# Optimization experiments

Measured on AMD Instinct MI355X. Metric: run time of the kernel, lower is better.

## Reference

```python
import jax, jax.numpy as jnp
from jax import lax
import numpy as np

SCORE_THRESH = 0.05
NMS_THRESH = 0.5
MAX_DET = 100
MIN_SIZE = 0.01
BBOX_CLIP = float(np.log(1000.0 / 16.0))
NEG = -1e10


def setup_inputs() -> dict:
    key = jax.random.key(0)
    ks = jax.random.split(key, 12)
    N, IN, REP, C = 2000, 256 * 7 * 7, 1024, 91
    box_features = jax.random.normal(ks[0], (N, IN), jnp.float32)
    x1 = jax.random.uniform(ks[1], (N,), jnp.float32, 0.0, 1000.0)
    y1 = jax.random.uniform(ks[2], (N,), jnp.float32, 0.0, 600.0)
    bw = jax.random.uniform(ks[3], (N,), jnp.float32, 16.0, 200.0)
    bh = jax.random.uniform(ks[4], (N,), jnp.float32, 16.0, 180.0)
    proposals = jnp.stack([x1, y1, x1 + bw, y1 + bh], axis=1)
    W1 = jax.random.normal(ks[5], (IN, REP), jnp.float32) * 0.01
    b1 = jnp.zeros((REP,), jnp.float32)
    W2 = jax.random.normal(ks[6], (REP, REP), jnp.float32) * 0.03
    b2 = jnp.zeros((REP,), jnp.float32)
    Wc = jax.random.normal(ks[7], (REP, C), jnp.float32) * 0.1
    bc = jax.random.normal(ks[8], (C,), jnp.float32) * 0.5
    Wr = jax.random.normal(ks[9], (REP, 4 * C), jnp.float32) * 0.01
    br = jnp.zeros((4 * C,), jnp.float32)
    return dict(box_features=box_features, proposals=proposals,
                W1=W1, b1=b1, W2=W2, b2=b2, Wc=Wc, bc=bc, Wr=Wr, br=br,
                image_h=800, image_w=1216)


def _nms(boxes, scores):
    """Greedy NMS with fixed trip count; scores already masked to NEG for invalid."""
    M = boxes.shape[0]
    areas = (boxes[:, 2] - boxes[:, 0]) * (boxes[:, 3] - boxes[:, 1])
    idxs = jnp.arange(M)

    def step(sm, _):
        i = jnp.argmax(sm)
        valid = sm[i] > NEG * 0.5
        b = boxes[i]
        xx1 = jnp.maximum(b[0], boxes[:, 0]); yy1 = jnp.maximum(b[1], boxes[:, 1])
        xx2 = jnp.minimum(b[2], boxes[:, 2]); yy2 = jnp.minimum(b[3], boxes[:, 3])
        inter = jnp.clip(xx2 - xx1, 0.0) * jnp.clip(yy2 - yy1, 0.0)
        iou = inter / (areas[i] + areas - inter + 1e-9)
        suppress = (iou > NMS_THRESH) | (idxs == i)
        sm = jnp.where(valid, jnp.where(suppress, NEG, sm), sm)
        return sm, jnp.where(valid, i, -1)

    _, keep = lax.scan(step, scores, None, length=MAX_DET)
    return keep  # [MAX_DET] int, -1 for padding


def reference(box_features, proposals, W1, b1, W2, b2, Wc, bc, Wr, br, image_h, image_w):
    N = box_features.shape[0]
    C = Wc.shape[1]
    # box head MLP (Linear+ReLU x2) and predictors
    h = jax.nn.relu(box_features @ W1 + b1)
    h = jax.nn.relu(h @ W2 + b2)
    class_logits = h @ Wc + bc                      # [N, C]
    box_reg = (h @ Wr + br).reshape(N, C, 4)        # [N, C, 4]
    # box decode (weights 10,10,5,5) against proposals
    pw = proposals[:, 2] - proposals[:, 0]
    ph = proposals[:, 3] - proposals[:, 1]
    pcx = proposals[:, 0] + 0.5 * pw
    pcy = proposals[:, 1] + 0.5 * ph
    dx = box_reg[..., 0] / 10.0
    dy = box_reg[..., 1] / 10.0
    dw = jnp.minimum(box_reg[..., 2] / 5.0, BBOX_CLIP)
    dh = jnp.minimum(box_reg[..., 3] / 5.0, BBOX_CLIP)
    cx = dx * pw[:, None] + pcx[:, None]
    cy = dy * ph[:, None] + pcy[:, None]
    w = jnp.exp(dw) * pw[:, None]
    hh = jnp.exp(dh) * ph[:, None]
    boxes = jnp.stack([cx - 0.5 * w, cy - 0.5 * hh, cx + 0.5 * w, cy + 0.5 * hh], axis=-1)
    scores = jax.nn.softmax(class_logits, axis=-1)
    # clip to image
    Wim = jnp.float32(image_w); Him = jnp.float32(image_h)
    boxes = jnp.stack([jnp.clip(boxes[..., 0], 0.0, Wim),
                       jnp.clip(boxes[..., 1], 0.0, Him),
                       jnp.clip(boxes[..., 2], 0.0, Wim),
                       jnp.clip(boxes[..., 3], 0.0, Him)], axis=-1)
    # drop background class, flatten to [N*(C-1)]
    boxes = boxes[:, 1:].reshape(-1, 4)
    scores = scores[:, 1:].reshape(-1)
    labels = jnp.broadcast_to(jnp.arange(1, C, dtype=jnp.int32), (N, C - 1)).reshape(-1)
    # score threshold + remove small boxes (as masking, static shapes)
    bw = boxes[:, 2] - boxes[:, 0]
    bh = boxes[:, 3] - boxes[:, 1]
    valid = (scores > SCORE_THRESH) & (bw >= MIN_SIZE) & (bh >= MIN_SIZE)
    sm = jnp.where(valid, scores, NEG)
    # class-aware (batched) NMS via per-class coordinate offsets
    off = labels.astype(boxes.dtype) * (jnp.maximum(Wim, Him) + 1.0)
    keep = _nms(boxes + off[:, None], sm)
    mask = keep >= 0
    idx = jnp.maximum(keep, 0)
    out_boxes = jnp.take(boxes, idx, axis=0) * mask[:, None]
    out_scores = jnp.take(scores, idx) * mask
    out_labels = jnp.take(labels, idx) * mask.astype(jnp.int32)
    return out_boxes, out_scores, out_labels
```

## Files before the change

kernel.cpp:

```cpp
#include <hip/hip_runtime.h>

#define CPC 2000
#define SPC 100
#define NCLS 90
#define TM 128
#define TN 128
#define TKK 16

typedef __attribute__((ext_vector_type(8))) short bf16x8;
typedef __attribute__((ext_vector_type(4))) float f32x4;

__device__ __forceinline__ unsigned short f2bf_rne(float f) {
    unsigned u = __float_as_uint(f);
    return (unsigned short)((u + 0x7FFFu + ((u >> 16) & 1u)) >> 16);
}
__device__ __forceinline__ unsigned short f2bf_trunc(float f) {
    return (unsigned short)(__float_as_uint(f) >> 16);
}
__device__ __forceinline__ float bfhi_f32(float f) {
    return __uint_as_float(__float_as_uint(f) & 0xFFFF0000u);
}
__device__ __forceinline__ void async_load16(const void* g, void* l) {
    __builtin_amdgcn_global_load_lds((const __attribute__((address_space(1))) unsigned int*)g,
                                     (__attribute__((address_space(3))) unsigned int*)l, 16, 0, 0);
}
__device__ __forceinline__ int swz(int c) { return c ^ ((c >> 3) & 3); }

__global__ __launch_bounds__(256) void split_transpose(
    const float* __restrict__ W, unsigned short* __restrict__ Thi,
    unsigned short* __restrict__ Tlo, int K, int N)
{
    __shared__ float tile[32][33];
    const int kt = blockIdx.x * 32, nt = blockIdx.y * 32;
    const int tx = threadIdx.x & 31, ty = threadIdx.x >> 5;
#pragma unroll
    for (int j = 0; j < 4; ++j) {
        int k = kt + ty + j * 8, n = nt + tx;
        tile[ty + j * 8][tx] = (k < K && n < N) ? W[(size_t)k * N + n] : 0.f;
    }
    __syncthreads();
#pragma unroll
    for (int j = 0; j < 4; ++j) {
        int n = nt + ty + j * 8, k = kt + tx;
        if (n < N && k < K) {
            float f = tile[tx][ty + j * 8];
            Thi[(size_t)n * K + k] = f2bf_trunc(f);
            Tlo[(size_t)n * K + k] = f2bf_rne(f - bfhi_f32(f));
        }
    }
}

__global__ __launch_bounds__(256) void split_transpose2(
    const float* __restrict__ Wa, const float* __restrict__ Wb, int Na, int Nb,
    unsigned short* __restrict__ Thi, unsigned short* __restrict__ Tlo, int K)
{
    const int N = Na + Nb;
    __shared__ float tile[32][33];
    const int kt = blockIdx.x * 32, nt = blockIdx.y * 32;
    const int tx = threadIdx.x & 31, ty = threadIdx.x >> 5;
#pragma unroll
    for (int j = 0; j < 4; ++j) {
        int k = kt + ty + j * 8, n = nt + tx;
        float v = 0.f;
        if (k < K && n < N)
            v = (n < Na) ? Wa[(size_t)k * Na + n] : Wb[(size_t)k * Nb + (n - Na)];
        tile[ty + j * 8][tx] = v;
    }
    __syncthreads();
#pragma unroll
    for (int j = 0; j < 4; ++j) {
        int n = nt + ty + j * 8, k = kt + tx;
        if (n < N && k < K) {
            float f = tile[tx][ty + j * 8];
            Thi[(size_t)n * K + k] = f2bf_trunc(f);
            Tlo[(size_t)n * K + k] = f2bf_rne(f - bfhi_f32(f));
        }
    }
}

__global__ __launch_bounds__(256, 4) void gemm_bf16x3_f32a(
    const float* __restrict__ A, const unsigned short* __restrict__ Bhi,
    const unsigned short* __restrict__ Blo, float* __restrict__ C,
    int M, int N, int K, int klen)
{
    __shared__ unsigned short Ah[2048], Al[2048], Bh[4096], Bl[4096];
    const int tid = threadIdx.x;
    const int wv = tid >> 6, ln = tid & 63;
    const int q = ln >> 4, lm = ln & 15;
    const int m0 = blockIdx.y * 64, n0 = blockIdx.x * 128;
    const int k0 = blockIdx.z * klen, k1 = k0 + klen;
    const int bcol_t = wv * 32;

    f32x4 acc[4][2];
#pragma unroll
    for (int i = 0; i < 4; ++i)
#pragma unroll
        for (int j = 0; j < 2; ++j) acc[i][j] = (f32x4)0.f;

    const int r = tid >> 2, h = tid & 3;
    int gr = m0 + r; if (gr >= M) gr = M - 1;
    const float* Arow = A + (size_t)gr * K + h * 8;
    const int apc = swz(tid);

    unsigned bsrc[2];
#pragma unroll
    for (int i = 0; i < 2; ++i) {
        int s = i * 256 + tid;
        int gn = n0 + (s >> 2); if (gn >= N) gn = N - 1;
        int qe = (s & 3) ^ ((s >> 3) & 3);
        bsrc[i] = (unsigned)gn * (unsigned)K + (unsigned)(qe * 8);
    }

    for (int kt = k0; kt < k1; kt += 32) {
#pragma unroll
        for (int i = 0; i < 2; ++i) {
            async_load16(Bhi + bsrc[i] + kt, &Bh[(i * 256 + wv * 64) * 8]);
            async_load16(Blo + bsrc[i] + kt, &Bl[(i * 256 + wv * 64) * 8]);
        }
        float4 v0 = *reinterpret_cast<const float4*>(Arow + kt);
        float4 v1 = *reinterpret_cast<const float4*>(Arow + kt + 4);
        float f[8] = {v0.x, v0.y, v0.z, v0.w, v1.x, v1.y, v1.z, v1.w};
        bf16x8 hi, lo;
#pragma unroll
        for (int e = 0; e < 8; ++e) {
            hi[e] = (short)f2bf_trunc(f[e]);
            lo[e] = (short)f2bf_rne(f[e] - bfhi_f32(f[e]));
        }
        *(bf16x8*)&Ah[apc * 8] = hi;
        *(bf16x8*)&Al[apc * 8] = lo;
        __syncthreads();

        bf16x8 afh[4], afl[4], bfh[2], bfl[2];
#pragma unroll
        for (int mi = 0; mi < 4; ++mi) {
            int p = swz((mi * 16 + lm) * 4 + q);
            afh[mi] = *(const bf16x8*)&Ah[p * 8];
            afl[mi] = *(const bf16x8*)&Al[p * 8];
        }
#pragma unroll
        for (int ni = 0; ni < 2; ++ni) {
            int p = swz((bcol_t + ni * 16 + lm) * 4 + q);
            bfh[ni] = *(const bf16x8*)&Bh[p * 8];
            bfl[ni] = *(const bf16x8*)&Bl[p * 8];
        }
#pragma unroll
        for (int mi = 0; mi < 4; ++mi)
#pragma unroll
            for (int ni = 0; ni < 2; ++ni) {
                acc[mi][ni] = __builtin_amdgcn_mfma_f32_16x16x32_bf16(afh[mi], bfh[ni], acc[mi][ni], 0, 0, 0);
                acc[mi][ni] = __builtin_amdgcn_mfma_f32_16x16x32_bf16(afl[mi], bfh[ni], acc[mi][ni], 0, 0, 0);
                acc[mi][ni] = __builtin_amdgcn_mfma_f32_16x16x32_bf16(afh[mi], bfl[ni], acc[mi][ni], 0, 0, 0);
            }
        __syncthreads();
    }

    float* Cz = C + (size_t)blockIdx.z * (size_t)M * (size_t)N;
#pragma unroll
    for (int mi = 0; mi < 4; ++mi)
#pragma unroll
        for (int ni = 0; ni < 2; ++ni)
#pragma unroll
            for (int ri = 0; ri < 4; ++ri) {
                int rr = m0 + mi * 16 + q * 4 + ri;
                int cc = n0 + bcol_t + ni * 16 + lm;
                if (rr < M && cc < N) Cz[(size_t)rr * N + cc] = acc[mi][ni][ri];
            }
}

__global__ __launch_bounds__(256, 4) void gemm_bf16x3_sa(
    const unsigned short* __restrict__ Ahi_g, const unsigned short* __restrict__ Alo_g,
    const unsigned short* __restrict__ Bhi, const unsigned short* __restrict__ Blo,
    float* __restrict__ C, int M, int N, int K, int klen)
{
    __shared__ unsigned short Ah[2048], Al[2048], Bh[4096], Bl[4096];
    const int tid = threadIdx.x;
    const int wv = tid >> 6, ln = tid & 63;
    const int q = ln >> 4, lm = ln & 15;
    const int m0 = blockIdx.y * 64, n0 = blockIdx.x * 128;
    const int k0 = blockIdx.z * klen, k1 = k0 + klen;
    const int bcol_t = wv * 32;

    f32x4 acc[4][2];
#pragma unroll
    for (int i = 0; i < 4; ++i)
#pragma unroll
        for (int j = 0; j < 2; ++j) acc[i][j] = (f32x4)0.f;

    {
    }
    int agr = m0 + (tid >> 2); if (agr >= M) agr = M - 1;
    const int aqe = (tid & 3) ^ ((tid >> 3) & 3);
    const unsigned asrc = (unsigned)agr * (unsigned)K + (unsigned)(aqe * 8);

    unsigned bsrc[2];
#pragma unroll
    for (int i = 0; i < 2; ++i) {
        int s = i * 256 + tid;
        int gn = n0 + (s >> 2); if (gn >= N) gn = N - 1;
        int qe = (s & 3) ^ ((s >> 3) & 3);
        bsrc[i] = (unsigned)gn * (unsigned)K + (unsigned)(qe * 8);
    }

    for (int kt = k0; kt < k1; kt += 32) {
        async_load16(Ahi_g + asrc + kt, &Ah[(wv * 64) * 8]);
        async_load16(Alo_g + asrc + kt, &Al[(wv * 64) * 8]);
#pragma unroll
        for (int i = 0; i < 2; ++i) {
            async_load16(Bhi + bsrc[i] + kt, &Bh[(i * 256 + wv * 64) * 8]);
            async_load16(Blo + bsrc[i] + kt, &Bl[(i * 256 + wv * 64) * 8]);
        }
        __syncthreads();

        bf16x8 afh[4], afl[4], bfh[2], bfl[2];
#pragma unroll
        for (int mi = 0; mi < 4; ++mi) {
            int p = swz((mi * 16 + lm) * 4 + q);
            afh[mi] = *(const bf16x8*)&Ah[p * 8];
            afl[mi] = *(const bf16x8*)&Al[p * 8];
        }
#pragma unroll
        for (int ni = 0; ni < 2; ++ni) {
            int p = swz((bcol_t + ni * 16 + lm) * 4 + q);
            bfh[ni] = *(const bf16x8*)&Bh[p * 8];
            bfl[ni] = *(const bf16x8*)&Bl[p * 8];
        }
#pragma unroll
        for (int mi = 0; mi < 4; ++mi)
#pragma unroll
            for (int ni = 0; ni < 2; ++ni) {
                acc[mi][ni] = __builtin_amdgcn_mfma_f32_16x16x32_bf16(afh[mi], bfh[ni], acc[mi][ni], 0, 0, 0);
                acc[mi][ni] = __builtin_amdgcn_mfma_f32_16x16x32_bf16(afl[mi], bfh[ni], acc[mi][ni], 0, 0, 0);
                acc[mi][ni] = __builtin_amdgcn_mfma_f32_16x16x32_bf16(afh[mi], bfl[ni], acc[mi][ni], 0, 0, 0);
            }
        __syncthreads();
    }

    float* Cz = C + (size_t)blockIdx.z * (size_t)M * (size_t)N;
#pragma unroll
    for (int mi = 0; mi < 4; ++mi)
#pragma unroll
        for (int ni = 0; ni < 2; ++ni)
#pragma unroll
            for (int ri = 0; ri < 4; ++ri) {
                int rr = m0 + mi * 16 + q * 4 + ri;
                int cc = n0 + bcol_t + ni * 16 + lm;
                if (rr < M && cc < N) Cz[(size_t)rr * N + cc] = acc[mi][ni][ri];
            }
}

__global__ __launch_bounds__(256) void gemm_f32(
    const float* __restrict__ A, const float* __restrict__ B,
    const float* __restrict__ bias, float* __restrict__ C,
    int M, int N, int K, int ksplit, int relu)
{
    __shared__ float As[TKK][TM + 4];
    __shared__ float Bs[TKK][TN + 4];
    const int tid = threadIdx.x;
    const int tx = tid & 15, ty = tid >> 4;
    const int m0 = blockIdx.y * TM, n0 = blockIdx.x * TN;
    const int z = blockIdx.z;
    const int kstart = z * ksplit;
    const int kend = (kstart + ksplit < K) ? (kstart + ksplit) : K;
    float* Cz = C + (size_t)z * (size_t)M * (size_t)N;
    const bool nvec = ((N & 3) == 0);

    float acc[8][8];
#pragma unroll
    for (int i = 0; i < 8; ++i)
#pragma unroll
        for (int j = 0; j < 8; ++j) acc[i][j] = 0.f;

    for (int kt = kstart; kt < kend; kt += TKK) {
#pragma unroll
        for (int l = 0; l < 2; ++l) {
            int idx = tid + l * 256;
            int rr = idx >> 2, kq = idx & 3;
            float4 v = make_float4(0.f, 0.f, 0.f, 0.f);
            int grr = m0 + rr;
            if (grr < M)
                v = *reinterpret_cast<const float4*>(A + (size_t)grr * K + kt + (kq << 2));
            As[(kq << 2) + 0][rr] = v.x;
            As[(kq << 2) + 1][rr] = v.y;
            As[(kq << 2) + 2][rr] = v.z;
            As[(kq << 2) + 3][rr] = v.w;
        }
#pragma unroll
        for (int l = 0; l < 2; ++l) {
            int idx = tid + l * 256;
            int kk = idx >> 5, nq = idx & 31;
            int gn = n0 + (nq << 2);
            const float* bp = B + (size_t)(kt + kk) * N + gn;
            float4 v;
            if (nvec && gn + 3 < N) {
                v = *reinterpret_cast<const float4*>(bp);
            } else {
                v.x = (gn + 0 < N) ? bp[0] : 0.f;
                v.y = (gn + 1 < N) ? bp[1] : 0.f;
                v.z = (gn + 2 < N) ? bp[2] : 0.f;
                v.w = (gn + 3 < N) ? bp[3] : 0.f;
            }
            *reinterpret_cast<float4*>(&Bs[kk][nq << 2]) = v;
        }
        __syncthreads();
#pragma unroll
        for (int kk = 0; kk < TKK; ++kk) {
            float a[8], b[8];
            *reinterpret_cast<float4*>(&a[0]) = *reinterpret_cast<const float4*>(&As[kk][ty * 8]);
            *reinterpret_cast<float4*>(&a[4]) = *reinterpret_cast<const float4*>(&As[kk][ty * 8 + 4]);
            *reinterpret_cast<float4*>(&b[0]) = *reinterpret_cast<const float4*>(&Bs[kk][tx * 4]);
            *reinterpret_cast<float4*>(&b[4]) = *reinterpret_cast<const float4*>(&Bs[kk][64 + tx * 4]);
#pragma unroll
            for (int i = 0; i < 8; ++i)
#pragma unroll
                for (int j = 0; j < 8; ++j)
                    acc[i][j] = fmaf(a[i], b[j], acc[i][j]);
        }
        __syncthreads();
    }
#pragma unroll
    for (int i = 0; i < 8; ++i) {
        int grr = m0 + ty * 8 + i;
        if (grr >= M) continue;
#pragma unroll
        for (int j = 0; j < 8; ++j) {
            int gc = n0 + ((j < 4) ? (tx * 4 + j) : (64 + tx * 4 + (j - 4)));
            if (gc >= N) continue;
            float v = acc[i][j];
            if (bias) v += bias[gc];
            if (relu) v = fmaxf(v, 0.f);
            Cz[(size_t)grr * N + gc] = v;
        }
    }
}

__global__ void combine_bias_act(const float* __restrict__ P, const float* __restrict__ bias,
                                 float* __restrict__ H, int total, int N, int nsplit,
                                 int pstride, int relu)
{
    int i = blockIdx.x * blockDim.x + threadIdx.x;
    if (i >= total) return;
    float s = P[i];
    for (int j = 1; j < nsplit; ++j) s += P[i + (size_t)j * (size_t)pstride];
    s += bias[i % N];
    if (relu) s = fmaxf(s, 0.f);
    H[i] = s;
}

__global__ void combine_bias_split(const float* __restrict__ P, const float* __restrict__ bias,
                                   unsigned short* __restrict__ Hhi, unsigned short* __restrict__ Hlo,
                                   int total, int N, int nsplit, int pstride, int relu)
{
    int i = blockIdx.x * blockDim.x + threadIdx.x;
    if (i >= total) return;
    float s = P[i];
    for (int j = 1; j < nsplit; ++j) s += P[i + (size_t)j * (size_t)pstride];
    s += bias[i % N];
    if (relu) s = fmaxf(s, 0.f);
    Hhi[i] = f2bf_trunc(s);
    Hlo[i] = f2bf_rne(s - bfhi_f32(s));
}

__global__ void combine_head(const float* __restrict__ P, const float* __restrict__ bc,
                             const float* __restrict__ br, float* __restrict__ H,
                             int total, int nsplit, int pstride)
{
    int i = blockIdx.x * blockDim.x + threadIdx.x;
    if (i >= total) return;
    float s = P[i];
    for (int j = 1; j < nsplit; ++j) s += P[i + (size_t)j * (size_t)pstride];
    int col = i % 455;
    s += (col < 91) ? bc[col] : br[col - 91];
    H[i] = s;
}

__device__ __forceinline__ float scalar_dim(const int* p)
{
    int iv = *p;
    return (iv > 0 && iv < (1 << 20)) ? (float)iv : *reinterpret_cast<const float*>(p);
}

__global__ __launch_bounds__(128) void decode_compact(
    const float* __restrict__ logits, int lstr, const float* __restrict__ breg, int bstr,
    const float4* __restrict__ proposals, const int* __restrict__ ihp,
    const int* __restrict__ iwp,
    float4* __restrict__ cbox, float* __restrict__ cscore, int* __restrict__ cn,
    int* __restrict__ ccnt)
{
    const int n = blockIdx.x;
    const int c = threadIdx.x;
    __shared__ float sl[91];
    __shared__ float s_max, s_sum;
    if (c < 91) sl[c] = logits[(size_t)n * lstr + c];
    __syncthreads();
    if (c == 0) {
        float m = sl[0];
        for (int i = 1; i < 91; ++i) m = fmaxf(m, sl[i]);
        float s = 0.f;
        for (int i = 0; i < 91; ++i) s += expf(sl[i] - m);
        s_max = m; s_sum = s;
    }
    __syncthreads();
    if (c < 1 || c >= 91) return;

    const float score = expf(sl[c] - s_max) / s_sum;
    const float Wim = scalar_dim(iwp), Him = scalar_dim(ihp);
    float4 p = proposals[n];
    float pw = p.z - p.x, ph = p.w - p.y;
    float pcx = p.x + 0.5f * pw, pcy = p.y + 0.5f * ph;
    const float* r4 = breg + (size_t)n * bstr + c * 4;
    float dxv = r4[0] / 10.f, dyv = r4[1] / 10.f;
    const float BCLIP = 4.135166556742356f;
    float dwv = fminf(r4[2] / 5.f, BCLIP);
    float dhv = fminf(r4[3] / 5.f, BCLIP);
    float cx = dxv * pw + pcx, cy = dyv * ph + pcy;
    float w = expf(dwv) * pw, hh = expf(dhv) * ph;
    float x1 = cx - 0.5f * w, y1 = cy - 0.5f * hh;
    float x2 = cx + 0.5f * w, y2 = cy + 0.5f * hh;
    x1 = fminf(fmaxf(x1, 0.f), Wim);
    y1 = fminf(fmaxf(y1, 0.f), Him);
    x2 = fminf(fmaxf(x2, 0.f), Wim);
    y2 = fminf(fmaxf(y2, 0.f), Him);
    float bw = x2 - x1, bh = y2 - y1;
    if (score > 0.05f && bw >= 0.01f && bh >= 0.01f) {
        int cls = c - 1;
        int pos = atomicAdd(&ccnt[cls], 1);
        if (pos < CPC) {
            cbox[cls * CPC + pos] = make_float4(x1, y1, x2, y2);
            cscore[cls * CPC + pos] = score;
            cn[cls * CPC + pos] = n;
        }
    }
}

__global__ __launch_bounds__(256) void nms_class(
    const float4* __restrict__ cbox, const float* __restrict__ cscore,
    const int* __restrict__ cn, const int* __restrict__ ccnt,
    float4* __restrict__ sbox, float* __restrict__ sscore,
    unsigned long long* __restrict__ skey, int* __restrict__ scnt)
{
    const int cls = blockIdx.x;
    const int tid = threadIdx.x;
    int cnt = ccnt[cls]; if (cnt > CPC) cnt = CPC;

    __shared__ float4 cb[CPC];
    __shared__ unsigned long long keys[CPC];
    __shared__ unsigned long long red[4];
    __shared__ float4 selsh;
    __shared__ int selidx_sh;

    for (int i = tid; i < cnt; i += 256) {
        cb[i] = cbox[cls * CPC + i];
        unsigned int sb = __float_as_uint(cscore[cls * CPC + i]);
        sb ^= (sb >> 31) ? 0xFFFFFFFFu : 0x80000000u;
        unsigned int flat = (unsigned)cn[cls * CPC + i] * 90u + (unsigned)cls;
        keys[i] = ((unsigned long long)sb << 32) | (unsigned long long)(0xFFFFFFFFu - flat);
    }
    __syncthreads();

    int sel = 0;
    while (sel < SPC) {
        unsigned long long best = 0ull;
        for (int i = tid; i < cnt; i += 256) {
            unsigned long long k = keys[i];
            if (k > best) best = k;
        }
#pragma unroll
        for (int d = 32; d >= 1; d >>= 1) {
            unsigned long long o = __shfl_down(best, d, 64);
            if (o > best) best = o;
        }
        if ((tid & 63) == 0) red[tid >> 6] = best;
        __syncthreads();
        unsigned long long gbest = red[0];
        if (red[1] > gbest) gbest = red[1];
        if (red[2] > gbest) gbest = red[2];
        if (red[3] > gbest) gbest = red[3];
        if (gbest == 0ull) break;
        for (int i = tid; i < cnt; i += 256)
            if (keys[i] == gbest) { selsh = cb[i]; selidx_sh = i; }
        __syncthreads();
        float4 s = selsh;
        const int si = selidx_sh;
        const float sa = (s.z - s.x) * (s.w - s.y);
        if (tid == 0) {
            sbox[cls * SPC + sel] = s;
            unsigned int sb = (unsigned int)(gbest >> 32);
            sb ^= (sb >> 31) ? 0x80000000u : 0xFFFFFFFFu;
            sscore[cls * SPC + sel] = __uint_as_float(sb);
            skey[cls * SPC + sel] = gbest;
        }
        for (int i = tid; i < cnt; i += 256) {
            float4 b = cb[i];
            float xx1 = fmaxf(s.x, b.x), yy1 = fmaxf(s.y, b.y);
            float xx2 = fminf(s.z, b.z), yy2 = fminf(s.w, b.w);
            float inter = fmaxf(xx2 - xx1, 0.f) * fmaxf(yy2 - yy1, 0.f);
            float area = (b.z - b.x) * (b.w - b.y);
            if (3.f * inter > sa + area + 1e-9f || i == si) keys[i] = 0ull;
        }
        ++sel;
        __syncthreads();
    }
    if (tid == 0) scnt[cls] = sel;
}

__global__ __launch_bounds__(128) void nms_merge(
    const float4* __restrict__ sbox, const float* __restrict__ sscore,
    const unsigned long long* __restrict__ skey, const int* __restrict__ scnt,
    float* __restrict__ out)
{
    const int tid = threadIdx.x;
    __shared__ int head[NCLS];
    __shared__ unsigned long long red[2];
    __shared__ int selc_sh;
    if (tid < NCLS) head[tid] = 0;
    __syncthreads();

    for (int k = 0; k < 100; ++k) {
        unsigned long long key = 0ull;
        if (tid < NCLS && head[tid] < scnt[tid]) key = skey[tid * SPC + head[tid]];
        unsigned long long mykey = key;
#pragma unroll
        for (int d = 32; d >= 1; d >>= 1) {
            unsigned long long o = __shfl_down(key, d, 64);
            if (o > key) key = o;
        }
        if ((tid & 63) == 0) red[tid >> 6] = key;
        if (tid == 0) selc_sh = -1;
        __syncthreads();
        unsigned long long gbest = red[0] > red[1] ? red[0] : red[1];
        if (gbest != 0ull && mykey == gbest) selc_sh = tid;
        __syncthreads();
        const int c = selc_sh;
        if (tid == 0) {
            if (c >= 0) {
                int h = head[c];
                float4 b = sbox[c * SPC + h];
                out[k * 4 + 0] = b.x; out[k * 4 + 1] = b.y;
                out[k * 4 + 2] = b.z; out[k * 4 + 3] = b.w;
                out[400 + k] = sscore[c * SPC + h];
                out[500 + k] = (float)(c + 1);
            } else {
                out[k * 4 + 0] = 0.f; out[k * 4 + 1] = 0.f;
                out[k * 4 + 2] = 0.f; out[k * 4 + 3] = 0.f;
                out[400 + k] = 0.f; out[500 + k] = 0.f;
            }
        }
        if (c >= 0 && tid == c) head[c]++;
        __syncthreads();
    }
}

extern "C" void kernel_launch(void* const* d_in, const int* in_sizes, int n_in,
                              void* d_out, int out_size, void* d_ws, size_t ws_size,
                              hipStream_t stream)
{
    const float* bf    = (const float*)d_in[0];
    const float* props = (const float*)d_in[1];
    const float* W1    = (const float*)d_in[2];
    const float* b1    = (const float*)d_in[3];
    const float* W2    = (const float*)d_in[4];
    const float* b2    = (const float*)d_in[5];
    const float* Wc    = (const float*)d_in[6];
    const float* bc    = (const float*)d_in[7];
    const float* Wr    = (const float*)d_in[8];
    const float* br    = (const float*)d_in[9];
    const int*   ihp   = (const int*)d_in[10];
    const int*   iwp   = (const int*)d_in[11];
    float* ws  = (float*)d_ws;
    float* out = (float*)d_out;

    const size_t MN   = 2000ull * 1024ull;
    const size_t NLOG = 2000ull * 91ull;
    const size_t NREG = 2000ull * 364ull;
    const size_t NHEAD = 2000ull * 455ull;
    const size_t ws_floats = ws_size / 4;

    const size_t BT1F = 1024ull * 12544ull / 2;
    const size_t WT2F = 1024ull * 1024ull / 2;
    const size_t WHF  = 455ull * 1024ull / 2;
    const size_t NMSF = (size_t)NCLS * CPC * 6 + (size_t)NCLS * SPC * 7 + 256;
    const size_t PF   = 4 * MN;
    const size_t NEED = 2 * BT1F + 2 * WT2F + 2 * WHF + 2 * MN + NHEAD + NMSF + PF + 64;

    if (ws_floats >= NEED) {
        unsigned short* BT1hi = (unsigned short*)ws;
        unsigned short* BT1lo = (unsigned short*)(ws + BT1F);
        unsigned short* WT2hi = (unsigned short*)(ws + 2 * BT1F);
        unsigned short* WT2lo = (unsigned short*)(ws + 2 * BT1F + WT2F);
        unsigned short* WHhi  = (unsigned short*)(ws + 2 * BT1F + 2 * WT2F);
        unsigned short* WHlo  = (unsigned short*)(ws + 2 * BT1F + 2 * WT2F + WHF);
        float* H1   = ws + 2 * BT1F + 2 * WT2F + 2 * WHF;
        float* H2   = H1 + MN;
        float* HEAD = H2 + MN;
        float* CBOX   = HEAD + NHEAD;
        float* CSCORE = CBOX + (size_t)NCLS * CPC * 4;
        int*   CN     = (int*)(CSCORE + (size_t)NCLS * CPC);
        float* SBOX   = (float*)(CN + (size_t)NCLS * CPC);
        float* SSCORE = SBOX + (size_t)NCLS * SPC * 4;
        unsigned long long* SKEY = (unsigned long long*)(SSCORE + (size_t)NCLS * SPC);
        int*   CCNT = (int*)(SKEY + (size_t)NCLS * SPC);
        int*   SCNT = CCNT + NCLS;
        float* P = (float*)(SCNT + NCLS + 62);

        unsigned short* H1hi = (unsigned short*)H1;
        unsigned short* H1lo = H1hi + MN;
        unsigned short* H2hi = (unsigned short*)H2;
        unsigned short* H2lo = H2hi + MN;

        split_transpose<<<dim3(392, 32), 256, 0, stream>>>(W1, BT1hi, BT1lo, 12544, 1024);
        split_transpose<<<dim3(32, 32), 256, 0, stream>>>(W2, WT2hi, WT2lo, 1024, 1024);
        split_transpose2<<<dim3(32, 15), 256, 0, stream>>>(Wc, Wr, 91, 364, WHhi, WHlo, 1024);
        gemm_bf16x3_f32a<<<dim3(8, 32, 4), 256, 0, stream>>>(bf, BT1hi, BT1lo, P,
                                                             2000, 1024, 12544, 3136);
        combine_bias_split<<<(int)((MN + 255) / 256), 256, 0, stream>>>(P, b1, H1hi, H1lo,
                                                             (int)MN, 1024, 4, (int)MN, 1);
        gemm_bf16x3_sa<<<dim3(8, 32, 4), 256, 0, stream>>>(H1hi, H1lo, WT2hi, WT2lo, P,
                                                           2000, 1024, 1024, 256);
        combine_bias_split<<<(int)((MN + 255) / 256), 256, 0, stream>>>(P, b2, H2hi, H2lo,
                                                             (int)MN, 1024, 4, (int)MN, 1);
        gemm_bf16x3_sa<<<dim3(4, 32, 8), 256, 0, stream>>>(H2hi, H2lo, WHhi, WHlo, P,
                                                           2000, 455, 1024, 128);
        combine_head<<<(int)((NHEAD + 255) / 256), 256, 0, stream>>>(P, bc, br, HEAD,
                                                             (int)NHEAD, 8, (int)NHEAD);
        hipMemsetAsync(CCNT, 0, 2 * NCLS * sizeof(int), stream);
        decode_compact<<<2000, 128, 0, stream>>>(HEAD, 455, HEAD + 91, 455,
                                                 (const float4*)props, ihp, iwp,
                                                 (float4*)CBOX, CSCORE, CN, CCNT);
        nms_class<<<NCLS, 256, 0, stream>>>((const float4*)CBOX, CSCORE, CN, CCNT,
                                            (float4*)SBOX, SSCORE, SKEY, SCNT);
        nms_merge<<<1, 128, 0, stream>>>((const float4*)SBOX, SSCORE, SKEY, SCNT, out);
        return;
    }

    const size_t NMSF2 = (size_t)NCLS * CPC * 6 + (size_t)NCLS * SPC * 7 + 256;
    const size_t TAILF = 2 * MN + NLOG + NREG + NMSF2;
    int z1 = 2;
    if (ws_floats >= TAILF + 8 * MN) z1 = 8;
    else if (ws_floats >= TAILF + 4 * MN) z1 = 4;
    const size_t REUSE = (size_t)z1 * MN;
    int zh = (REUSE >= 8 * NREG) ? 8 : 4;

    float* P      = ws;
    float* H1     = P + REUSE;
    float* H2     = H1 + MN;
    float* LOG    = H2 + MN;
    float* BREG   = LOG + NLOG;
    float* CBOX   = BREG + NREG;
    float* CSCORE = CBOX + (size_t)NCLS * CPC * 4;
    int*   CN     = (int*)(CSCORE + (size_t)NCLS * CPC);
    float* SBOX   = (float*)(CN + (size_t)NCLS * CPC);
    float* SSCORE = SBOX + (size_t)NCLS * SPC * 4;
    unsigned long long* SKEY = (unsigned long long*)(SSCORE + (size_t)NCLS * SPC);
    int*   CCNT   = (int*)(SKEY + (size_t)NCLS * SPC);
    int*   SCNT   = CCNT + NCLS;

    gemm_f32<<<dim3(8, 16, z1), 256, 0, stream>>>(bf, W1, nullptr, P,
                                                  2000, 1024, 12544, 12544 / z1, 0);
    combine_bias_act<<<(int)((MN + 255) / 256), 256, 0, stream>>>(P, b1, H1,
                                                  (int)MN, 1024, z1, (int)MN, 1);
    gemm_f32<<<dim3(8, 16, 4), 256, 0, stream>>>(H1, W2, nullptr, P,
                                                 2000, 1024, 1024, 256, 0);
    combine_bias_act<<<(int)((MN + 255) / 256), 256, 0, stream>>>(P, b2, H2,
                                                 (int)MN, 1024, 4, (int)MN, 1);
    gemm_f32<<<dim3(1, 16, zh), 256, 0, stream>>>(H2, Wc, nullptr, P,
                                                  2000, 91, 1024, 1024 / zh, 0);
    combine_bias_act<<<(int)((NLOG + 255) / 256), 256, 0, stream>>>(P, bc, LOG,
                                                  (int)NLOG, 91, zh, (int)NLOG, 0);
    gemm_f32<<<dim3(3, 16, zh), 256, 0, stream>>>(H2, Wr, nullptr, P,
                                                  2000, 364, 1024, 1024 / zh, 0);
    combine_bias_act<<<(int)((NREG + 255) / 256), 256, 0, stream>>>(P, br, BREG,
                                                  (int)NREG, 364, zh, (int)NREG, 0);
    hipMemsetAsync(CCNT, 0, 2 * NCLS * sizeof(int), stream);
    decode_compact<<<2000, 128, 0, stream>>>(LOG, 91, BREG, 364,
                                             (const float4*)props, ihp, iwp,
                                             (float4*)CBOX, CSCORE, CN, CCNT);
    nms_class<<<NCLS, 256, 0, stream>>>((const float4*)CBOX, CSCORE, CN, CCNT,
                                        (float4*)SBOX, SSCORE, SKEY, SCNT);
    nms_merge<<<1, 128, 0, stream>>>((const float4*)SBOX, SSCORE, SKEY, SCNT, out);
}
```

Measured before the change: 751.0 us.

## Retune split-K counts, vectorize combine/transposes, raise GEMM occupancy, parallelize softmax

Changes the split-K factors of the three GEMMs (6, 5 and 6 splits with a clamped k1) and raises the launch bounds from 4 to 6 blocks per SM. The transpose-split kernels now handle 64 k-rows per block and write packed pairs of bf16 values. The combine kernels load and store float4 vectors. The softmax max/sum in decode moves from a single thread to tree reductions in shared memory. Workspace buffers are aliased so they fit the larger partial-sum buffers, and it is easy to get the liveness of these aliases wrong. The higher launch bound can also force register spills.

```diff
diff --git a/kernel.cpp b/kernel.cpp
--- a/kernel.cpp
+++ b/kernel.cpp
@@ -9,6 +9,7 @@
 
 typedef __attribute__((ext_vector_type(8))) short bf16x8;
 typedef __attribute__((ext_vector_type(4))) float f32x4;
+typedef __attribute__((ext_vector_type(4))) unsigned short u16x4;
 
 __device__ __forceinline__ unsigned short f2bf_rne(float f) {
     unsigned u = __float_as_uint(f);
@@ -30,22 +31,27 @@
     const float* __restrict__ W, unsigned short* __restrict__ Thi,
     unsigned short* __restrict__ Tlo, int K, int N)
 {
-    __shared__ float tile[32][33];
-    const int kt = blockIdx.x * 32, nt = blockIdx.y * 32;
+    __shared__ float tile[64][33];
+    const int kt = blockIdx.x * 64, nt = blockIdx.y * 32;
     const int tx = threadIdx.x & 31, ty = threadIdx.x >> 5;
 #pragma unroll
-    for (int j = 0; j < 4; ++j) {
+    for (int j = 0; j < 8; ++j) {
         int k = kt + ty + j * 8, n = nt + tx;
         tile[ty + j * 8][tx] = (k < K && n < N) ? W[(size_t)k * N + n] : 0.f;
     }
     __syncthreads();
 #pragma unroll
     for (int j = 0; j < 4; ++j) {
-        int n = nt + ty + j * 8, k = kt + tx;
+        int n = nt + ty + j * 8;
+        int k = kt + tx * 2;
         if (n < N && k < K) {
-            float f = tile[tx][ty + j * 8];
-            Thi[(size_t)n * K + k] = f2bf_trunc(f);
-            Tlo[(size_t)n * K + k] = f2bf_rne(f - bfhi_f32(f));
+            float f0 = tile[tx * 2][ty + j * 8];
+            float f1 = tile[tx * 2 + 1][ty + j * 8];
+            unsigned hi = (unsigned)f2bf_trunc(f0) | ((unsigned)f2bf_trunc(f1) << 16);
+            unsigned lo = (unsigned)f2bf_rne(f0 - bfhi_f32(f0))
+                        | ((unsigned)f2bf_rne(f1 - bfhi_f32(f1)) << 16);
+            *reinterpret_cast<unsigned*>(&Thi[(size_t)n * K + k]) = hi;
+            *reinterpret_cast<unsigned*>(&Tlo[(size_t)n * K + k]) = lo;
         }
     }
 }
@@ -55,11 +61,11 @@
     unsigned short* __restrict__ Thi, unsigned short* __restrict__ Tlo, int K)
 {
     const int N = Na + Nb;
-    __shared__ float tile[32][33];
-    const int kt = blockIdx.x * 32, nt = blockIdx.y * 32;
+    __shared__ float tile[64][33];
+    const int kt = blockIdx.x * 64, nt = blockIdx.y * 32;
     const int tx = threadIdx.x & 31, ty = threadIdx.x >> 5;
 #pragma unroll
-    for (int j = 0; j < 4; ++j) {
+    for (int j = 0; j < 8; ++j) {
         int k = kt + ty + j * 8, n = nt + tx;
         float v = 0.f;
         if (k < K && n < N)
@@ -69,16 +75,21 @@
     __syncthreads();
 #pragma unroll
     for (int j = 0; j < 4; ++j) {
-        int n = nt + ty + j * 8, k = kt + tx;
+        int n = nt + ty + j * 8;
+        int k = kt + tx * 2;
         if (n < N && k < K) {
-            float f = tile[tx][ty + j * 8];
-            Thi[(size_t)n * K + k] = f2bf_trunc(f);
-            Tlo[(size_t)n * K + k] = f2bf_rne(f - bfhi_f32(f));
-        }
-    }
-}
-
-__global__ __launch_bounds__(256, 4) void gemm_bf16x3_f32a(
+            float f0 = tile[tx * 2][ty + j * 8];
+            float f1 = tile[tx * 2 + 1][ty + j * 8];
+            unsigned hi = (unsigned)f2bf_trunc(f0) | ((unsigned)f2bf_trunc(f1) << 16);
+            unsigned lo = (unsigned)f2bf_rne(f0 - bfhi_f32(f0))
+                        | ((unsigned)f2bf_rne(f1 - bfhi_f32(f1)) << 16);
+            *reinterpret_cast<unsigned*>(&Thi[(size_t)n * K + k]) = hi;
+            *reinterpret_cast<unsigned*>(&Tlo[(size_t)n * K + k]) = lo;
+        }
+    }
+}
+
+__global__ __launch_bounds__(256, 6) void gemm_bf16x3_f32a(
     const float* __restrict__ A, const unsigned short* __restrict__ Bhi,
     const unsigned short* __restrict__ Blo, float* __restrict__ C,
     int M, int N, int K, int klen)
@@ -88,7 +99,8 @@
     const int wv = tid >> 6, ln = tid & 63;
     const int q = ln >> 4, lm = ln & 15;
     const int m0 = blockIdx.y * 64, n0 = blockIdx.x * 128;
-    const int k0 = blockIdx.z * klen, k1 = k0 + klen;
+    const int k0 = blockIdx.z * klen;
+    int k1 = k0 + klen; if (k1 > K) k1 = K;
     const int bcol_t = wv * 32;
 
     f32x4 acc[4][2];
@@ -97,9 +109,8 @@
 #pragma unroll
         for (int j = 0; j < 2; ++j) acc[i][j] = (f32x4)0.f;
 
-    const int r = tid >> 2, h = tid & 3;
-    int gr = m0 + r; if (gr >= M) gr = M - 1;
-    const float* Arow = A + (size_t)gr * K + h * 8;
+    int gr = m0 + (tid >> 2); if (gr >= M) gr = M - 1;
+    const float* Arow = A + (size_t)gr * K + (tid & 3) * 8;
     const int apc = swz(tid);
 
     unsigned bsrc[2];
@@ -167,7 +178,7 @@
             }
 }
 
-__global__ __launch_bounds__(256, 4) void gemm_bf16x3_sa(
+__global__ __launch_bounds__(256, 6) void gemm_bf16x3_sa(
     const unsigned short* __restrict__ Ahi_g, const unsigned short* __restrict__ Alo_g,
     const unsigned short* __restrict__ Bhi, const unsigned short* __restrict__ Blo,
     float* __restrict__ C, int M, int N, int K, int klen)
@@ -177,7 +188,8 @@
     const int wv = tid >> 6, ln = tid & 63;
     const int q = ln >> 4, lm = ln & 15;
     const int m0 = blockIdx.y * 64, n0 = blockIdx.x * 128;
-    const int k0 = blockIdx.z * klen, k1 = k0 + klen;
+    const int k0 = blockIdx.z * klen;
+    int k1 = k0 + klen; if (k1 > K) k1 = K;
     const int bcol_t = wv * 32;
 
     f32x4 acc[4][2];
@@ -186,11 +198,9 @@
 #pragma unroll
         for (int j = 0; j < 2; ++j) acc[i][j] = (f32x4)0.f;
 
-    {
-    }
     int agr = m0 + (tid >> 2); if (agr >= M) agr = M - 1;
-    const int aqe = (tid & 3) ^ ((tid >> 3) & 3);
-    const unsigned asrc = (unsigned)agr * (unsigned)K + (unsigned)(aqe * 8);
+    const unsigned asrc = (unsigned)agr * (unsigned)K
+                        + (unsigned)(((tid & 3) ^ ((tid >> 3) & 3)) * 8);
 
     unsigned bsrc[2];
 #pragma unroll
@@ -350,27 +360,44 @@
                                    unsigned short* __restrict__ Hhi, unsigned short* __restrict__ Hlo,
                                    int total, int N, int nsplit, int pstride, int relu)
 {
-    int i = blockIdx.x * blockDim.x + threadIdx.x;
+    int i = (blockIdx.x * blockDim.x + threadIdx.x) * 4;
     if (i >= total) return;
-    float s = P[i];
-    for (int j = 1; j < nsplit; ++j) s += P[i + (size_t)j * (size_t)pstride];
-    s += bias[i % N];
-    if (relu) s = fmaxf(s, 0.f);
-    Hhi[i] = f2bf_trunc(s);
-    Hlo[i] = f2bf_rne(s - bfhi_f32(s));
+    float4 s = *reinterpret_cast<const float4*>(P + i);
+    for (int j = 1; j < nsplit; ++j) {
+        float4 p = *reinterpret_cast<const float4*>(P + i + (size_t)j * (size_t)pstride);
+        s.x += p.x; s.y += p.y; s.z += p.z; s.w += p.w;
+    }
+    const float4 b = *reinterpret_cast<const float4*>(bias + (i % N));
+    s.x += b.x; s.y += b.y; s.z += b.z; s.w += b.w;
+    if (relu) {
+        s.x = fmaxf(s.x, 0.f); s.y = fmaxf(s.y, 0.f);
+        s.z = fmaxf(s.z, 0.f); s.w = fmaxf(s.w, 0.f);
+    }
+    u16x4 hi = { f2bf_trunc(s.x), f2bf_trunc(s.y), f2bf_trunc(s.z), f2bf_trunc(s.w) };
+    u16x4 lo = { f2bf_rne(s.x - bfhi_f32(s.x)), f2bf_rne(s.y - bfhi_f32(s.y)),
+                 f2bf_rne(s.z - bfhi_f32(s.z)), f2bf_rne(s.w - bfhi_f32(s.w)) };
+    *reinterpret_cast<u16x4*>(&Hhi[i]) = hi;
+    *reinterpret_cast<u16x4*>(&Hlo[i]) = lo;
 }
 
 __global__ void combine_head(const float* __restrict__ P, const float* __restrict__ bc,
                              const float* __restrict__ br, float* __restrict__ H,
                              int total, int nsplit, int pstride)
 {
-    int i = blockIdx.x * blockDim.x + threadIdx.x;
+    int i = (blockIdx.x * blockDim.x + threadIdx.x) * 4;
     if (i >= total) return;
-    float s = P[i];
-    for (int j = 1; j < nsplit; ++j) s += P[i + (size_t)j * (size_t)pstride];
-    int col = i % 455;
-    s += (col < 91) ? bc[col] : br[col - 91];
-    H[i] = s;
+    float4 s = *reinterpret_cast<const float4*>(P + i);
+    for (int j = 1; j < nsplit; ++j) {
+        float4 p = *reinterpret_cast<const float4*>(P + i + (size_t)j * (size_t)pstride);
+        s.x += p.x; s.y += p.y; s.z += p.z; s.w += p.w;
+    }
+    float sv[4] = {s.x, s.y, s.z, s.w};
+#pragma unroll
+    for (int e = 0; e < 4; ++e) {
+        int col = (i + e) % 455;
+        sv[e] += (col < 91) ? bc[col] : br[col - 91];
+    }
+    *reinterpret_cast<float4*>(&H[i]) = make_float4(sv[0], sv[1], sv[2], sv[3]);
 }
 
 __device__ __forceinline__ float scalar_dim(const int* p)
@@ -389,17 +416,26 @@
     const int n = blockIdx.x;
     const int c = threadIdx.x;
     __shared__ float sl[91];
-    __shared__ float s_max, s_sum;
+    __shared__ float red[128];
     if (c < 91) sl[c] = logits[(size_t)n * lstr + c];
     __syncthreads();
-    if (c == 0) {
-        float m = sl[0];
-        for (int i = 1; i < 91; ++i) m = fmaxf(m, sl[i]);
-        float s = 0.f;
-        for (int i = 0; i < 91; ++i) s += expf(sl[i] - m);
-        s_max = m; s_sum = s;
-    }
+    red[c] = (c < 91) ? sl[c] : -3.0e38f;
     __syncthreads();
+#pragma unroll
+    for (int s = 64; s > 0; s >>= 1) {
+        if (c < s) red[c] = fmaxf(red[c], red[c + s]);
+        __syncthreads();
+    }
+    const float s_max = red[0];
+    __syncthreads();
+    red[c] = (c < 91) ? expf(sl[c] - s_max) : 0.f;
+    __syncthreads();
+#pragma unroll
+    for (int s = 64; s > 0; s >>= 1) {
+        if (c < s) red[c] += red[c + s];
+        __syncthreads();
+    }
+    const float s_sum = red[0];
     if (c < 1 || c >= 91) return;
 
     const float score = expf(sl[c] - s_max) / s_sum;
@@ -589,10 +625,15 @@
         unsigned short* WT2lo = (unsigned short*)(ws + 2 * BT1F + WT2F);
         unsigned short* WHhi  = (unsigned short*)(ws + 2 * BT1F + 2 * WT2F);
         unsigned short* WHlo  = (unsigned short*)(ws + 2 * BT1F + 2 * WT2F + WHF);
-        float* H1   = ws + 2 * BT1F + 2 * WT2F + 2 * WHF;
-        float* H2   = H1 + MN;
-        float* HEAD = H2 + MN;
-        float* CBOX   = HEAD + NHEAD;
+        float* T = ws + 2 * BT1F + 2 * WT2F + 2 * WHF;
+
+        float* H1   = T;
+        float* P1   = T + MN;
+        float* P2   = T + MN;
+        float* H2   = T + 6 * MN;
+        float* P3   = T;
+        float* HEAD = T + 7 * MN;
+        float* CBOX   = T;
         float* CSCORE = CBOX + (size_t)NCLS * CPC * 4;
         int*   CN     = (int*)(CSCORE + (size_t)NCLS * CPC);
         float* SBOX   = (float*)(CN + (size_t)NCLS * CPC);
@@ -600,28 +641,27 @@
         unsigned long long* SKEY = (unsigned long long*)(SSCORE + (size_t)NCLS * SPC);
         int*   CCNT = (int*)(SKEY + (size_t)NCLS * SPC);
         int*   SCNT = CCNT + NCLS;
-        float* P = (float*)(SCNT + NCLS + 62);
 
         unsigned short* H1hi = (unsigned short*)H1;
         unsigned short* H1lo = H1hi + MN;
         unsigned short* H2hi = (unsigned short*)H2;
         unsigned short* H2lo = H2hi + MN;
 
-        split_transpose<<<dim3(392, 32), 256, 0, stream>>>(W1, BT1hi, BT1lo, 12544, 1024);
-        split_transpose<<<dim3(32, 32), 256, 0, stream>>>(W2, WT2hi, WT2lo, 1024, 1024);
-        split_transpose2<<<dim3(32, 15), 256, 0, stream>>>(Wc, Wr, 91, 364, WHhi, WHlo, 1024);
-        gemm_bf16x3_f32a<<<dim3(8, 32, 4), 256, 0, stream>>>(bf, BT1hi, BT1lo, P,
-                                                             2000, 1024, 12544, 3136);
-        combine_bias_split<<<(int)((MN + 255) / 256), 256, 0, stream>>>(P, b1, H1hi, H1lo,
-                                                             (int)MN, 1024, 4, (int)MN, 1);
-        gemm_bf16x3_sa<<<dim3(8, 32, 4), 256, 0, stream>>>(H1hi, H1lo, WT2hi, WT2lo, P,
-                                                           2000, 1024, 1024, 256);
-        combine_bias_split<<<(int)((MN + 255) / 256), 256, 0, stream>>>(P, b2, H2hi, H2lo,
-                                                             (int)MN, 1024, 4, (int)MN, 1);
-        gemm_bf16x3_sa<<<dim3(4, 32, 8), 256, 0, stream>>>(H2hi, H2lo, WHhi, WHlo, P,
-                                                           2000, 455, 1024, 128);
-        combine_head<<<(int)((NHEAD + 255) / 256), 256, 0, stream>>>(P, bc, br, HEAD,
-                                                             (int)NHEAD, 8, (int)NHEAD);
+        split_transpose<<<dim3(196, 32), 256, 0, stream>>>(W1, BT1hi, BT1lo, 12544, 1024);
+        split_transpose<<<dim3(16, 32), 256, 0, stream>>>(W2, WT2hi, WT2lo, 1024, 1024);
+        split_transpose2<<<dim3(16, 15), 256, 0, stream>>>(Wc, Wr, 91, 364, WHhi, WHlo, 1024);
+        gemm_bf16x3_f32a<<<dim3(8, 32, 6), 256, 0, stream>>>(bf, BT1hi, BT1lo, P1,
+                                                             2000, 1024, 12544, 2112);
+        combine_bias_split<<<(int)(MN / 4 / 256), 256, 0, stream>>>(P1, b1, H1hi, H1lo,
+                                                             (int)MN, 1024, 6, (int)MN, 1);
+        gemm_bf16x3_sa<<<dim3(8, 32, 5), 256, 0, stream>>>(H1hi, H1lo, WT2hi, WT2lo, P2,
+                                                           2000, 1024, 1024, 224);
+        combine_bias_split<<<(int)(MN / 4 / 256), 256, 0, stream>>>(P2, b2, H2hi, H2lo,
+                                                             (int)MN, 1024, 5, (int)MN, 1);
+        gemm_bf16x3_sa<<<dim3(4, 32, 6), 256, 0, stream>>>(H2hi, H2lo, WHhi, WHlo, P3,
+                                                           2000, 455, 1024, 192);
+        combine_head<<<(int)((NHEAD / 4 + 255) / 256), 256, 0, stream>>>(P3, bc, br, HEAD,
+                                                             (int)NHEAD, 6, (int)NHEAD);
         hipMemsetAsync(CCNT, 0, 2 * NCLS * sizeof(int), stream);
         decode_compact<<<2000, 128, 0, stream>>>(HEAD, 455, HEAD + 91, 455,
                                                  (const float4*)props, ihp, iwp,
```

Result: slower. 830.6 us (+10.6%).
